# Kernel tuning notes

Hardware: AMD Instinct MI355X
Metric: run time of the kernel (lower is better)

The kernel has to match this reference:

```python
import jax, jax.numpy as jnp
import numpy as np

NUM_FEATURES = 256
NUM_PIDS = 5532
CQ_SIZE = 5000
N_NONID = 256
N = 2048
OIM_SCALAR = 30.0
MOMENTUM = 0.5


def _unit_rows(key, shape):
    v = jax.random.normal(key, shape, dtype=jnp.float32)
    return v / jnp.linalg.norm(v, axis=-1, keepdims=True)


def setup_inputs() -> dict:
    key = jax.random.key(0)
    ks = jax.random.split(key, 8)
    inputs = _unit_rows(ks[0], (N, NUM_FEATURES))
    targets = jax.random.randint(ks[1], (N,), 0, NUM_PIDS + 100, dtype=jnp.int32)
    belong_to_first_half = jax.random.randint(ks[2], (N,), 0, 2) > 0
    non_id_feat = _unit_rows(ks[3], (N_NONID, NUM_FEATURES))
    lut = _unit_rows(ks[4], (NUM_PIDS, NUM_FEATURES))
    cq = _unit_rows(ks[5], (CQ_SIZE, NUM_FEATURES))
    first_pos_sample = _unit_rows(ks[6], (NUM_PIDS, NUM_FEATURES))
    second_pos_sample = _unit_rows(ks[7], (NUM_PIDS, NUM_FEATURES))
    return {
        "inputs": inputs,
        "non_id_feat": non_id_feat,
        "lut": lut,
        "cq": cq,
        "first_pos_sample": first_pos_sample,
        "second_pos_sample": second_pos_sample,
        "targets": targets,
        "belong_to_first_half": belong_to_first_half,
        "header": 0,
    }


def reference(inputs, non_id_feat, lut, cq, first_pos_sample, second_pos_sample,
              targets, belong_to_first_half, header):
    # OIM forward: similarities against labeled LUT and [circular queue; non-id feats]
    out_labeled = inputs @ lut.T                                  # [N, num_pids]
    out_unlabeled = inputs @ jnp.concatenate([cq, non_id_feat], 0).T  # [N, cq+nonid]
    projected = jnp.concatenate([out_labeled, out_unlabeled], axis=1)
    return projected * OIM_SCALAR
```

## Files before the change

### kernel.cpp

```cpp
#include <hip/hip_runtime.h>
#include <hip/hip_bf16.h>
#include <stdint.h>
#include <stddef.h>

#define NUM_FEATURES 256
#define NUM_PIDS 5532
#define CQ_SIZE 5000
#define N_NONID 256
#define N_ROWS 2048
#define N_COLS (NUM_PIDS + CQ_SIZE + N_NONID)
#define OIM_SCALAR 30.0f

#define BM 128
#define BN 128
#define BK 32
#define KITERS (NUM_FEATURES / BK)

#define NT_PER_XCD 11
#define N_TILES 85
#define M_TILES 16
#define GRID_BLOCKS (8 * NT_PER_XCD * M_TILES)

typedef __bf16 bf16_t;
typedef __bf16 bf16x4 __attribute__((ext_vector_type(4)));
typedef __bf16 bf16x8 __attribute__((ext_vector_type(8)));
typedef float f32x4 __attribute__((ext_vector_type(4)));

__global__ __launch_bounds__(256)
void oim_gemm_kernel(const float* __restrict__ A,
                     const float* __restrict__ lut,
                     const float* __restrict__ cq,
                     const float* __restrict__ nonid,
                     float* __restrict__ out) {
    __shared__ __align__(16) bf16_t As[2][BM * BK];
    __shared__ __align__(16) bf16_t Bs[2][BM * BK];

    const int id  = blockIdx.x;
    const int xcd = id & 7;
    const int l   = id >> 3;
    const int nt  = xcd * NT_PER_XCD + l % NT_PER_XCD;
    const int mt  = l / NT_PER_XCD;
    if (nt >= N_TILES) return;
    const int m0 = mt * BM;
    const int n0 = nt * BN;

    const int tid  = threadIdx.x;
    const int wid  = tid >> 6;
    const int lane = tid & 63;

    const int srow = tid >> 3;
    const int skk  = (tid & 7) * 4;

    const float* arow[4];
    const float* brow[4];
    #pragma unroll
    for (int j = 0; j < 4; ++j) {
        const int rm = m0 + srow + j * 32;
        arow[j] = A + (size_t)rm * NUM_FEATURES + skk;
        int r = n0 + srow + j * 32;
        r = r < (N_COLS - 1) ? r : (N_COLS - 1);
        const float* src;
        if (r < NUM_PIDS)                 src = lut   + (size_t)r * NUM_FEATURES;
        else if (r < NUM_PIDS + CQ_SIZE)  src = cq    + (size_t)(r - NUM_PIDS) * NUM_FEATURES;
        else                              src = nonid + (size_t)(r - NUM_PIDS - CQ_SIZE) * NUM_FEATURES;
        brow[j] = src + skk;
    }

    const int wave_m = (wid >> 1) * 64;
    const int wave_n = (wid & 1) * 64;
    const int fr = lane & 15;
    const int fk = (lane >> 4) * 8;

    f32x4 acc[4][4] = {};

    float4 areg[4], breg[4];
    #pragma unroll
    for (int j = 0; j < 4; ++j) {
        areg[j] = *(const float4*)arow[j];
        breg[j] = *(const float4*)brow[j];
        arow[j] += BK;
        brow[j] += BK;
    }

    #pragma unroll 2
    for (int kt = 0; kt < KITERS; ++kt) {
        bf16_t* const as = As[kt & 1];
        bf16_t* const bs = Bs[kt & 1];
        #pragma unroll
        for (int j = 0; j < 4; ++j) {
            const int ldix = (srow + j * 32) * BK + skk;
            bf16x4 ac = { (bf16_t)areg[j].x, (bf16_t)areg[j].y,
                          (bf16_t)areg[j].z, (bf16_t)areg[j].w };
            bf16x4 bc = { (bf16_t)breg[j].x, (bf16_t)breg[j].y,
                          (bf16_t)breg[j].z, (bf16_t)breg[j].w };
            *(bf16x4*)&as[ldix] = ac;
            *(bf16x4*)&bs[ldix] = bc;
        }
        __syncthreads();
        if (kt < KITERS - 1) {
            #pragma unroll
            for (int j = 0; j < 4; ++j) {
                areg[j] = *(const float4*)arow[j];
                breg[j] = *(const float4*)brow[j];
                arow[j] += BK;
                brow[j] += BK;
            }
        }
        bf16x8 af[4], bfr[4];
        #pragma unroll
        for (int t = 0; t < 4; ++t) {
            af[t]  = *(const bf16x8*)&as[(wave_m + t * 16 + fr) * BK + fk];
            bfr[t] = *(const bf16x8*)&bs[(wave_n + t * 16 + fr) * BK + fk];
        }
        #pragma unroll
        for (int tm = 0; tm < 4; ++tm)
            #pragma unroll
            for (int tn = 0; tn < 4; ++tn)
                acc[tm][tn] = __builtin_amdgcn_mfma_f32_16x16x32_bf16(
                    af[tm], bfr[tn], acc[tm][tn], 0, 0, 0);
    }

    #pragma unroll
    for (int tm = 0; tm < 4; ++tm) {
        const int row_base = m0 + wave_m + tm * 16 + (lane >> 4) * 4;
        #pragma unroll
        for (int tn = 0; tn < 4; ++tn) {
            const int col = n0 + wave_n + tn * 16 + (lane & 15);
            if (col < N_COLS) {
                #pragma unroll
                for (int i = 0; i < 4; ++i) {
                    out[(size_t)(row_base + i) * N_COLS + col] =
                        acc[tm][tn][i] * OIM_SCALAR;
                }
            }
        }
    }
}

extern "C" void kernel_launch(void* const* d_in, const int* in_sizes, int n_in,
                              void* d_out, int out_size, void* d_ws, size_t ws_size,
                              hipStream_t stream) {
    const float* inputs = (const float*)d_in[0];
    const float* nonid  = (const float*)d_in[1];
    const float* lut    = (const float*)d_in[2];
    const float* cq     = (const float*)d_in[3];
    float* out = (float*)d_out;

    oim_gemm_kernel<<<dim3(GRID_BLOCKS), 256, 0, stream>>>(inputs, lut, cq, nonid, out);
}
```

Measured before the change: 147.5 us.

## Drop LDS staging; each wave loads MFMA fragments directly from global memory

Replaces the block-cooperative LDS double-buffered 128x128 tile with independent per-wave 64x64 tiles whose MFMA operands are read from global memory and converted to bf16 in registers. This removes shared-memory traffic and barriers, raises occupancy with a launch bound of two blocks, and switches to a simple 2D grid without the XCD-aware mapping. Output stores become nontemporal to avoid polluting cache with the large result. The tradeoff is less operand reuse per block and strided, less coalesced global loads that rely on L2/L1 to absorb redundant reads.

```diff
diff --git a/kernel.cpp b/kernel.cpp
--- a/kernel.cpp
+++ b/kernel.cpp
@@ -10,107 +10,69 @@
 #define N_ROWS 2048
 #define N_COLS (NUM_PIDS + CQ_SIZE + N_NONID)
 #define OIM_SCALAR 30.0f
+#define KITERS (NUM_FEATURES / 32)
 
-#define BM 128
-#define BN 128
-#define BK 32
-#define KITERS (NUM_FEATURES / BK)
-
-#define NT_PER_XCD 11
-#define N_TILES 85
-#define M_TILES 16
-#define GRID_BLOCKS (8 * NT_PER_XCD * M_TILES)
 
 typedef __bf16 bf16_t;
-typedef __bf16 bf16x4 __attribute__((ext_vector_type(4)));
 typedef __bf16 bf16x8 __attribute__((ext_vector_type(8)));
 typedef float f32x4 __attribute__((ext_vector_type(4)));
 
-__global__ __launch_bounds__(256)
+#define NT_WAVES ((N_COLS + 63) / 64)
+#define NBLK ((NT_WAVES + 3) / 4)
+#define MBLK (N_ROWS / 64)
+
+__global__ __launch_bounds__(256, 2)
 void oim_gemm_kernel(const float* __restrict__ A,
                      const float* __restrict__ lut,
                      const float* __restrict__ cq,
                      const float* __restrict__ nonid,
                      float* __restrict__ out) {
-    __shared__ __align__(16) bf16_t As[2][BM * BK];
-    __shared__ __align__(16) bf16_t Bs[2][BM * BK];
-
-    const int id  = blockIdx.x;
-    const int xcd = id & 7;
-    const int l   = id >> 3;
-    const int nt  = xcd * NT_PER_XCD + l % NT_PER_XCD;
-    const int mt  = l / NT_PER_XCD;
-    if (nt >= N_TILES) return;
-    const int m0 = mt * BM;
-    const int n0 = nt * BN;
-
     const int tid  = threadIdx.x;
-    const int wid  = tid >> 6;
+    const int w    = tid >> 6;
     const int lane = tid & 63;
 
-    const int srow = tid >> 3;
-    const int skk  = (tid & 7) * 4;
+    const int nt = blockIdx.x * 4 + w;
+    if (nt >= NT_WAVES) return;
+    const int m0 = blockIdx.y * 64;
+    const int n0 = nt * 64;
+
+    const int fr = lane & 15;
+    const int fk = (lane >> 4) * 8;
 
     const float* arow[4];
     const float* brow[4];
     #pragma unroll
-    for (int j = 0; j < 4; ++j) {
-        const int rm = m0 + srow + j * 32;
-        arow[j] = A + (size_t)rm * NUM_FEATURES + skk;
-        int r = n0 + srow + j * 32;
-        r = r < (N_COLS - 1) ? r : (N_COLS - 1);
+    for (int t = 0; t < 4; ++t) {
+        arow[t] = A + (size_t)(m0 + t * 16 + fr) * NUM_FEATURES + fk;
+        int r = n0 + t * 16 + fr;
+        r = r < N_COLS ? r : (N_COLS - 1);
         const float* src;
         if (r < NUM_PIDS)                 src = lut   + (size_t)r * NUM_FEATURES;
         else if (r < NUM_PIDS + CQ_SIZE)  src = cq    + (size_t)(r - NUM_PIDS) * NUM_FEATURES;
         else                              src = nonid + (size_t)(r - NUM_PIDS - CQ_SIZE) * NUM_FEATURES;
-        brow[j] = src + skk;
+        brow[t] = src + fk;
     }
-
-    const int wave_m = (wid >> 1) * 64;
-    const int wave_n = (wid & 1) * 64;
-    const int fr = lane & 15;
-    const int fk = (lane >> 4) * 8;
 
     f32x4 acc[4][4] = {};
 
-    float4 areg[4], breg[4];
     #pragma unroll
-    for (int j = 0; j < 4; ++j) {
-        areg[j] = *(const float4*)arow[j];
-        breg[j] = *(const float4*)brow[j];
-        arow[j] += BK;
-        brow[j] += BK;
-    }
-
-    #pragma unroll 2
-    for (int kt = 0; kt < KITERS; ++kt) {
-        bf16_t* const as = As[kt & 1];
-        bf16_t* const bs = Bs[kt & 1];
-        #pragma unroll
-        for (int j = 0; j < 4; ++j) {
-            const int ldix = (srow + j * 32) * BK + skk;
-            bf16x4 ac = { (bf16_t)areg[j].x, (bf16_t)areg[j].y,
-                          (bf16_t)areg[j].z, (bf16_t)areg[j].w };
-            bf16x4 bc = { (bf16_t)breg[j].x, (bf16_t)breg[j].y,
-                          (bf16_t)breg[j].z, (bf16_t)breg[j].w };
-            *(bf16x4*)&as[ldix] = ac;
-            *(bf16x4*)&bs[ldix] = bc;
-        }
-        __syncthreads();
-        if (kt < KITERS - 1) {
-            #pragma unroll
-            for (int j = 0; j < 4; ++j) {
-                areg[j] = *(const float4*)arow[j];
-                breg[j] = *(const float4*)brow[j];
-                arow[j] += BK;
-                brow[j] += BK;
-            }
-        }
-        bf16x8 af[4], bfr[4];
+    for (int kk = 0; kk < KITERS; ++kk) {
+        bf16x8 bfr[4], af[4];
         #pragma unroll
         for (int t = 0; t < 4; ++t) {
-            af[t]  = *(const bf16x8*)&as[(wave_m + t * 16 + fr) * BK + fk];
-            bfr[t] = *(const bf16x8*)&bs[(wave_n + t * 16 + fr) * BK + fk];
+            float4 b0 = *(const float4*)(brow[t]);
+            float4 b1 = *(const float4*)(brow[t] + 4);
+            brow[t] += 32;
+            bfr[t] = bf16x8{(bf16_t)b0.x, (bf16_t)b0.y, (bf16_t)b0.z, (bf16_t)b0.w,
+                            (bf16_t)b1.x, (bf16_t)b1.y, (bf16_t)b1.z, (bf16_t)b1.w};
+        }
+        #pragma unroll
+        for (int t = 0; t < 4; ++t) {
+            float4 a0 = *(const float4*)(arow[t]);
+            float4 a1 = *(const float4*)(arow[t] + 4);
+            arow[t] += 32;
+            af[t] = bf16x8{(bf16_t)a0.x, (bf16_t)a0.y, (bf16_t)a0.z, (bf16_t)a0.w,
+                           (bf16_t)a1.x, (bf16_t)a1.y, (bf16_t)a1.z, (bf16_t)a1.w};
         }
         #pragma unroll
         for (int tm = 0; tm < 4; ++tm)
@@ -122,15 +84,16 @@
 
     #pragma unroll
     for (int tm = 0; tm < 4; ++tm) {
-        const int row_base = m0 + wave_m + tm * 16 + (lane >> 4) * 4;
+        const int row_base = m0 + tm * 16 + (lane >> 4) * 4;
         #pragma unroll
         for (int tn = 0; tn < 4; ++tn) {
-            const int col = n0 + wave_n + tn * 16 + (lane & 15);
+            const int col = n0 + tn * 16 + fr;
             if (col < N_COLS) {
                 #pragma unroll
                 for (int i = 0; i < 4; ++i) {
-                    out[(size_t)(row_base + i) * N_COLS + col] =
-                        acc[tm][tn][i] * OIM_SCALAR;
+                    __builtin_nontemporal_store(
+                        acc[tm][tn][i] * OIM_SCALAR,
+                        &out[(size_t)(row_base + i) * N_COLS + col]);
                 }
             }
         }
@@ -146,5 +109,5 @@
     const float* cq     = (const float*)d_in[3];
     float* out = (float*)d_out;
 
-    oim_gemm_kernel<<<dim3(GRID_BLOCKS), 256, 0, stream>>>(inputs, lut, cq, nonid, out);
+    oim_gemm_kernel<<<dim3(NBLK, MBLK), 256, 0, stream>>>(inputs, lut, cq, nonid, out);
 }
```

Result: slower. 245.1 us (+66.2%).
